# Kernel tuning notes

Measured on AMD Instinct MI355X. Metric: run time of the kernel, lower is better.

## Reference

```python
import jax, jax.numpy as jnp
import numpy as np

B, C, H, W = 32, 3, 256, 256
NGN = 5  # MAX_NUM_OF_GN


def setup_inputs() -> dict:
    key = jax.random.key(0)
    ks = jax.random.split(key, 9)
    f_inp = jax.random.normal(ks[0], (B, C, H, W), jnp.float32)
    # pose: small rotation vector, translation with z ~ 1 (in front of camera)
    rvec = 0.1 * jax.random.normal(ks[1], (B, 3), jnp.float32)
    t_xy = 0.02 * jax.random.normal(ks[2], (B, 2), jnp.float32)
    t_z = 1.0 + 0.2 * jax.random.uniform(ks[3], (B, 1), jnp.float32)
    x_ini = jnp.concatenate([rvec, t_xy, t_z], axis=-1)  # (B,6)
    depth_map = 0.5 + jax.random.uniform(ks[4], (B, H, W), jnp.float32)
    face_index_map = jax.random.randint(ks[5], (B, H, W), 0, 50, jnp.int32) - 1  # -1 = background
    fx = fy = 572.4
    cx, cy = 325.3, 242.0
    Kmat = jnp.array([[fx, 0.0, cx], [0.0, fy, cy], [0.0, 0.0, 1.0]], jnp.float32)
    K = jnp.broadcast_to(Kmat, (B, 3, 3))
    bbox = jax.random.randint(ks[6], (B, 2), 0, 100, jnp.int32).astype(jnp.float32)
    W_pose = 0.1 * jax.random.normal(ks[7], (3, 6), jnp.float32)
    base_feat = jax.random.normal(ks[8], (1, C, H, W), jnp.float32)
    lam = jnp.full((1,), 0.1, jnp.float32)
    return dict(f_inp=f_inp, x_ini=x_ini, depth_map=depth_map,
                face_index_map=face_index_map, K=K, bbox=bbox,
                W_pose=W_pose, base_feat=base_feat, lam=lam)


def _render(x, W_pose, base_feat):
    # surrogate differentiable renderer: pose-conditioned feature map (B,C,H,W)
    return base_feat + jnp.tanh(x @ W_pose.T)[:, :, None, None]


def _spatial_gradient(f):
    # f: (B,C,H,W) -> (B,H,W,C,2) central differences (dx, dy)
    gx = jnp.gradient(f, axis=3)
    gy = jnp.gradient(f, axis=2)
    g = jnp.stack([gx, gy], axis=-1)          # (B,C,H,W,2)
    return jnp.transpose(g, (0, 2, 3, 1, 4))  # (B,H,W,C,2)


def _calculate_jacobian(depth, mask, K, t, bbox):
    # per-pixel 2x6 Jacobian of pixel projection wrt (rot_vec, t); (B,H,W,2,6)
    b, h, w = depth.shape
    fx = K[:, 0, 0][:, None, None]
    fy = K[:, 1, 1][:, None, None]
    cx = K[:, 0, 2][:, None, None]
    cy = K[:, 1, 2][:, None, None]
    u = bbox[:, 0][:, None, None] + jnp.arange(w, dtype=depth.dtype)[None, None, :]
    v = bbox[:, 1][:, None, None] + jnp.arange(h, dtype=depth.dtype)[None, :, None]
    z = depth
    xc = (u - cx) * z / fx            # backprojected camera-frame point
    yc = (v - cy) * z / fy
    zero = jnp.zeros_like(z)
    inv_z = 1.0 / z
    # projection Jacobian wrt camera-frame point: (B,H,W,2,3)
    Jp = jnp.stack([
        jnp.stack([fx * inv_z * jnp.ones_like(z), zero, -fx * xc * inv_z * inv_z], axis=-1),
        jnp.stack([zero, fy * inv_z * jnp.ones_like(z), -fy * yc * inv_z * inv_z], axis=-1),
    ], axis=-2)
    # rotated object point P = X_cam - t ; dX_cam/d(rot_vec) = -[P]_x
    px = xc - t[:, 0][:, None, None]
    py = yc - t[:, 1][:, None, None]
    pz = z - t[:, 2][:, None, None]
    S = jnp.stack([
        jnp.stack([zero, -pz, py], axis=-1),
        jnp.stack([pz, zero, -px], axis=-1),
        jnp.stack([-py, px, zero], axis=-1),
    ], axis=-2)                                       # (B,H,W,3,3)
    J_rot = -jnp.einsum('bhwij,bhwjk->bhwik', Jp, S)  # (B,H,W,2,3)
    Jc = jnp.concatenate([J_rot, Jp], axis=-1)        # (B,H,W,2,6)
    return Jc * mask[..., None, None]


def _gn_step(x, f_inp, depth_map, mask, K, bbox, W_pose, base_feat, damping):
    b = x.shape[0]
    f_rend = _render(x, W_pose, base_feat)                       # (B,C,H,W)
    e = jnp.transpose(f_inp - f_rend, (0, 2, 3, 1)).reshape(b, -1)  # (B, H*W*C)
    grad_xy = _spatial_gradient(f_rend)                          # (B,H,W,C,2)
    Jc = _calculate_jacobian(depth_map, mask, K, x[:, 3:], bbox)  # (B,H,W,2,6)
    J = jnp.einsum('bhwcx,bhwxs->bhwcs', grad_xy, Jc)            # (B,H,W,C,6)
    Jf = J.reshape(b, -1, 6)                                     # (B, H*W*C, 6)
    JtJ = jnp.einsum('bnc,bnd->bcd', Jf, Jf) + damping * jnp.eye(6, dtype=x.dtype)
    Jte = jnp.einsum('bnc,bn->bc', Jf, e)
    dx = jnp.linalg.solve(JtJ, Jte[..., None])[..., 0]
    return x + dx


def reference(f_inp, x_ini, depth_map, face_index_map, K, bbox, W_pose, base_feat, lam):
    mask = (face_index_map >= 0).astype(f_inp.dtype)  # valid rendered pixels
    damping = jax.nn.softplus(lam[0]) + 1e-6
    x = x_ini
    for _ in range(NGN):
        x = _gn_step(x, f_inp, depth_map, mask, K, bbox, W_pose, base_feat, damping)
    return x  # (B,6): refined (rot_vec, t)
```

## Files before the change

kernel.cpp:

```cpp
#include <hip/hip_runtime.h>
#include <math.h>

#define BATCH 32
#define CCH 3
#define HH 256
#define WW 256
#define HW (HH*WW)
#define NGN_IT 5
#define NM 45
#define TROWS 4
#define NTILE (HH/TROWS)
#define NTHR 256
#define NROWCP 38

__host__ __device__ constexpr int idxA(int i, int j) { return 6*i - i*(i+1)/2 + j; }

typedef __attribute__((address_space(1))) const unsigned int gu32;
typedef __attribute__((address_space(3))) unsigned int lu32;

__device__ __forceinline__ void gload_lds16(const float* g, float* l) {
    __builtin_amdgcn_global_load_lds((gu32*)g, (lu32*)l, 16, 0, 0);
}

template<int CTRL, int RMASK, int BMASK>
__device__ __forceinline__ float dpp_add(float x) {
    const int y = __builtin_amdgcn_update_dpp(0, __float_as_int(x), CTRL, RMASK, BMASK, true);
    return x + __int_as_float(y);
}
__device__ __forceinline__ float wave_sum(float x) {
    x = dpp_add<0x111, 0xf, 0xf>(x);
    x = dpp_add<0x112, 0xf, 0xf>(x);
    x = dpp_add<0x114, 0xf, 0xe>(x);
    x = dpp_add<0x118, 0xf, 0xc>(x);
    x = dpp_add<0x142, 0xa, 0xf>(x);
    x = dpp_add<0x143, 0xc, 0xf>(x);
    return x;
}

__global__ __launch_bounds__(NTHR, 4) void k_moments(
    const float* __restrict__ f_inp, const float* __restrict__ depth,
    const int* __restrict__ fidx, const float* __restrict__ Kmat,
    const float* __restrict__ bbox, const float* __restrict__ base_feat,
    float* __restrict__ partials)
{
    const int b   = blockIdx.y;
    const int h0  = blockIdx.x * TROWS;
    const int tid = threadIdx.x;

    __shared__ float bf_s [CCH][TROWS+2][WW];
    __shared__ float fin_s[CCH][TROWS][WW];
    __shared__ float dpt_s[TROWS][WW];
    __shared__ int   msk_s[TROWS][WW];
    __shared__ float red[4*NM];

    const int wv = tid >> 6, ln = tid & 63;

    for (int o = wv; o < NROWCP; o += 4) {
        const float* src; float* dst;
        if (o < 18) {
            const int c = o / 6, k = o % 6;
            int srow = h0 - 1 + k;
            srow = srow < 0 ? 0 : (srow > HH-1 ? HH-1 : srow);
            src = base_feat + ((size_t)c*HH + srow)*WW;
            dst = &bf_s[c][k][0];
        } else if (o < 30) {
            const int t = o - 18, c = t >> 2, r = t & 3;
            src = f_inp + (size_t)b*CCH*HW + ((size_t)c*HH + h0 + r)*WW;
            dst = &fin_s[c][r][0];
        } else if (o < 34) {
            const int r = o - 30;
            src = depth + (size_t)b*HW + (size_t)(h0 + r)*WW;
            dst = &dpt_s[r][0];
        } else {
            const int r = o - 34;
            src = (const float*)(fidx + (size_t)b*HW + (size_t)(h0 + r)*WW);
            dst = (float*)&msk_s[r][0];
        }
        gload_lds16(src + ln*4, dst);
    }

    const float fxv = Kmat[b*9+0], fyv = Kmat[b*9+4];
    const float cx  = Kmat[b*9+2], cy  = Kmat[b*9+5];
    const float bb0 = bbox[b*2+0], bb1 = bbox[b*2+1];
    const float ifx = __builtin_amdgcn_rcpf(fxv);
    const float ify = __builtin_amdgcn_rcpf(fyv);

    __syncthreads();

    const int lp = tid * 4;
    const int lr = lp >> 8;
    const int w0 = lp & (WW-1);
    const int h  = h0 + lr;

    const float4 zv = *(const float4*)&dpt_s[lr][w0];
    const int4   mv = *(const int4*)&msk_s[lr][w0];
    float iz[4];
    iz[0] = __builtin_amdgcn_rcpf(zv.x);
    iz[1] = __builtin_amdgcn_rcpf(zv.y);
    iz[2] = __builtin_amdgcn_rcpf(zv.z);
    iz[3] = __builtin_amdgcn_rcpf(zv.w);
    float mq[4];
    mq[0] = mv.x >= 0 ? 1.f : 0.f; mq[1] = mv.y >= 0 ? 1.f : 0.f;
    mq[2] = mv.z >= 0 ? 1.f : 0.f; mq[3] = mv.w >= 0 ? 1.f : 0.f;

    const float dv_ = bb1 + (float)h - cy;
    const float sy  = (h == 0 || h == HH-1) ? 1.0f : 0.5f;
    const float dvf = dv_*ify;
    const float r02 = -fxv*dvf;
    const float r10 = -(fyv + dv_*dvf);
    const float dvx = dv_*ifx;
    const float fyx = fyv*ifx;
    const float duB = bb0 + (float)w0 - cx;
    const float sx0 = (w0 == 0)    ? 1.0f : 0.5f;
    const float sx3 = (w0 == WW-4) ? 1.0f : 0.5f;
    const int wl = (w0 == 0)    ? 0    : w0-1;
    const int wr = (w0 == WW-4) ? WW-1 : w0+4;

    float acc[NM];
    #pragma unroll
    for (int k = 0; k < NM; ++k) acc[k] = 0.f;

    #pragma unroll
    for (int c = 0; c < CCH; ++c) {
        const float4 ct = *(const float4*)&bf_s[c][lr+1][w0];
        const float4 up = *(const float4*)&bf_s[c][lr+2][w0];
        const float4 dn = *(const float4*)&bf_s[c][lr  ][w0];
        const float lf = bf_s[c][lr+1][wl];
        const float rt = bf_s[c][lr+1][wr];
        const float4 fvc = *(const float4*)&fin_s[c][lr][w0];
        #pragma unroll
        for (int j = 0; j < 4; ++j) {
            const float gx  = (j==0) ? (ct.y - lf  )*sx0 :
                              (j==1) ? (ct.z - ct.x)*0.5f :
                              (j==2) ? (ct.w - ct.y)*0.5f :
                                       (rt   - ct.z)*sx3;
            const float gyv = ((j==0) ? (up.x - dn.x) :
                               (j==1) ? (up.y - dn.y) :
                               (j==2) ? (up.z - dn.z) :
                                        (up.w - dn.w)) * sy;
            const float fc  = (j==0) ? fvc.x : (j==1) ? fvc.y : (j==2) ? fvc.z : fvc.w;
            const float ctj = (j==0) ? ct.x  : (j==1) ? ct.y  : (j==2) ? ct.z  : ct.w;
            const float d   = fc - ctj;
            const float gxm = gx  * mq[j];
            const float gym = gyv * mq[j];
            const float du  = duB + (float)j;
            const float izj = iz[j];
            float J0[6];
            J0[0] = gxm*(-du*dvf)            + gym*r10;
            J0[1] = gxm*(fxv + du*du*ifx)    + gym*(du*dvx);
            J0[2] = gxm*r02                  + gym*(du*fyx);
            J0[3] = gxm*(fxv*izj);
            J0[4] = gym*(fyv*izj);
            J0[5] = -(gxm*du + gym*dv_)*izj;
            #pragma unroll
            for (int i = 0; i < 6; ++i)
                #pragma unroll
                for (int jj = i; jj < 6; ++jj)
                    acc[idxA(i,jj)] += J0[i]*J0[jj];
            #pragma unroll
            for (int s = 0; s < 6; ++s) acc[21 + s] += J0[s]*d;
            #pragma unroll
            for (int s = 0; s < 6; ++s) acc[27 + c*6 + s] += J0[s];
        }
    }

    #pragma unroll
    for (int k = 0; k < NM; ++k) {
        const float v = wave_sum(acc[k]);
        if (ln == 63) red[wv*NM + k] = v;
    }
    __syncthreads();
    if (tid < NM) {
        float s = red[tid] + red[NM + tid] + red[2*NM + tid] + red[3*NM + tid];
        partials[((size_t)b*NM + tid)*NTILE + blockIdx.x] = s;
    }
}

__global__ __launch_bounds__(64) void k_solve(
    const float* __restrict__ partials,
    const float* __restrict__ x_ini,
    const float* __restrict__ W_pose,
    const float* __restrict__ lam,
    float* __restrict__ out)
{
    const int b = blockIdx.x;
    const int tid = threadIdx.x;
    __shared__ float mom[NM];

    if (tid < NM) {
        const float* p = partials + ((size_t)b*NM + tid)*NTILE;
        double s = 0.0;
        #pragma unroll
        for (int i = 0; i < NTILE; ++i) s += (double)p[i];
        mom[tid] = (float)s;
    }
    __syncthreads();
    if (tid != 0) return;

    float A[6][6];
    for (int i = 0; i < 6; ++i)
        for (int j = i; j < 6; ++j) { float v = mom[idxA(i,j)]; A[i][j] = v; A[j][i] = v; }
    float q0[6];
    for (int s = 0; s < 6; ++s) q0[s] = mom[21 + s];
    float R0[3][6];
    for (int c = 0; c < 3; ++c) for (int s = 0; s < 6; ++s) R0[c][s] = mom[27 + c*6 + s];
    float Wp[3][6];
    for (int c = 0; c < 3; ++c) for (int s = 0; s < 6; ++s) Wp[c][s] = W_pose[c*6 + s];
    float x[6];
    for (int s = 0; s < 6; ++s) x[s] = x_ini[b*6 + s];
    const float damping = log1pf(expf(lam[0])) + 1e-6f;

    for (int it = 0; it < NGN_IT; ++it) {
        float tau[3];
        #pragma unroll
        for (int c = 0; c < 3; ++c) {
            float a = 0.f;
            #pragma unroll
            for (int s = 0; s < 6; ++s) a += x[s]*Wp[c][s];
            tau[c] = tanhf(a);
        }
        const float t0 = x[3], t1 = x[4], t2 = x[5];
        const float S[3][3] = {{0.f, -t2, t1}, {t2, 0.f, -t0}, {-t1, t0, 0.f}};

        float M[6][7];
        float PS[3][3], BS[3][3];
        #pragma unroll
        for (int i = 0; i < 3; ++i)
            #pragma unroll
            for (int j = 0; j < 3; ++j) {
                float s1 = 0.f, s2 = 0.f;
                #pragma unroll
                for (int k = 0; k < 3; ++k) { s1 += A[i][3+k]*S[k][j]; s2 += A[3+i][3+k]*S[k][j]; }
                PS[i][j] = s1; BS[i][j] = s2;
            }
        #pragma unroll
        for (int i = 0; i < 3; ++i)
            #pragma unroll
            for (int j = 0; j < 3; ++j) {
                float st = 0.f;
                #pragma unroll
                for (int k = 0; k < 3; ++k) st += S[k][i]*BS[k][j];
                M[i][j] = A[i][j] + PS[i][j] + PS[j][i] + st;
            }
        #pragma unroll
        for (int i = 0; i < 3; ++i)
            #pragma unroll
            for (int j = 0; j < 3; ++j) {
                float tr = A[i][3+j];
                #pragma unroll
                for (int k = 0; k < 3; ++k) tr += S[k][i]*A[3+k][3+j];
                M[i][3+j] = tr; M[3+j][i] = tr;
            }
        #pragma unroll
        for (int i = 0; i < 3; ++i)
            #pragma unroll
            for (int j = 0; j < 3; ++j) M[3+i][3+j] = A[3+i][3+j];
        #pragma unroll
        for (int d_ = 0; d_ < 6; ++d_) M[d_][d_] += damping;

        float base[6];
        #pragma unroll
        for (int s = 0; s < 6; ++s) {
            float v = q0[s];
            #pragma unroll
            for (int c = 0; c < 3; ++c) v -= tau[c]*R0[c][s];
            base[s] = v;
        }
        #pragma unroll
        for (int s = 0; s < 3; ++s) {
            float v = base[s];
            #pragma unroll
            for (int k = 0; k < 3; ++k) v += S[k][s]*base[3+k];
            M[s][6] = v;
        }
        #pragma unroll
        for (int s = 3; s < 6; ++s) M[s][6] = base[s];

        #pragma unroll
        for (int col = 0; col < 6; ++col) {
            const float inv = 1.0f / M[col][col];
            #pragma unroll
            for (int r = col+1; r < 6; ++r) {
                const float f = M[r][col]*inv;
                #pragma unroll
                for (int cc = col; cc < 7; ++cc) M[r][cc] -= f*M[col][cc];
            }
        }
        float sol[6];
        #pragma unroll
        for (int r = 5; r >= 0; --r) {
            float s = M[r][6];
            #pragma unroll
            for (int cc = r+1; cc < 6; ++cc) s -= M[r][cc]*sol[cc];
            sol[r] = s / M[r][r];
        }
        #pragma unroll
        for (int s = 0; s < 6; ++s) x[s] += sol[s];
    }
    #pragma unroll
    for (int s = 0; s < 6; ++s) out[b*6 + s] = x[s];
}

extern "C" void kernel_launch(void* const* d_in, const int* in_sizes, int n_in,
                              void* d_out, int out_size, void* d_ws, size_t ws_size,
                              hipStream_t stream)
{
    (void)in_sizes; (void)n_in; (void)out_size; (void)ws_size;
    const float* f_inp = (const float*)d_in[0];
    const float* x_ini = (const float*)d_in[1];
    const float* depth = (const float*)d_in[2];
    const int*   fidx  = (const int*)  d_in[3];
    const float* Kmat  = (const float*)d_in[4];
    const float* bbox  = (const float*)d_in[5];
    const float* Wp    = (const float*)d_in[6];
    const float* bfeat = (const float*)d_in[7];
    const float* lam   = (const float*)d_in[8];
    float* out = (float*)d_out;

    float* partials = (float*)d_ws;

    dim3 gB(NTILE, BATCH);
    k_moments<<<gB, NTHR, 0, stream>>>(f_inp, depth, fidx, Kmat, bbox, bfeat, partials);
    k_solve<<<BATCH, 64, 0, stream>>>(partials, x_ini, Wp, lam, out);
}
```

Measured before the change: 33.54 us.

## Replace LDS staging with direct global loads and two quads per thread

Drops the async global-to-LDS staging of base_feat, f_inp, depth and mask rows and the barrier that followed it. Each thread now reads its float4s and stencil neighbours straight from global memory, relying on cache for the halo rows. Each block handles 8 rows in two iterations, which halves the grid and the number of partials k_solve must sum. The cost is redundant neighbour loads served from L1/L2 instead of LDS, and fewer blocks to hide load latency.

New measurement: 131.7 us. +292.5%, slower.

```diff
diff --git a/kernel.cpp b/kernel.cpp
--- a/kernel.cpp
+++ b/kernel.cpp
@@ -8,19 +8,11 @@
 #define HW (HH*WW)
 #define NGN_IT 5
 #define NM 45
-#define TROWS 4
-#define NTILE (HH/TROWS)
+#define NBLK 32
 #define NTHR 256
-#define NROWCP 38
+#define QPT 2
 
 __host__ __device__ constexpr int idxA(int i, int j) { return 6*i - i*(i+1)/2 + j; }
-
-typedef __attribute__((address_space(1))) const unsigned int gu32;
-typedef __attribute__((address_space(3))) unsigned int lu32;
-
-__device__ __forceinline__ void gload_lds16(const float* g, float* l) {
-    __builtin_amdgcn_global_load_lds((gu32*)g, (lu32*)l, 16, 0, 0);
-}
 
 template<int CTRL, int RMASK, int BMASK>
 __device__ __forceinline__ float dpp_add(float x) {
@@ -44,40 +36,11 @@
     float* __restrict__ partials)
 {
     const int b   = blockIdx.y;
-    const int h0  = blockIdx.x * TROWS;
+    const int blk = blockIdx.x;
     const int tid = threadIdx.x;
 
-    __shared__ float bf_s [CCH][TROWS+2][WW];
-    __shared__ float fin_s[CCH][TROWS][WW];
-    __shared__ float dpt_s[TROWS][WW];
-    __shared__ int   msk_s[TROWS][WW];
     __shared__ float red[4*NM];
-
     const int wv = tid >> 6, ln = tid & 63;
-
-    for (int o = wv; o < NROWCP; o += 4) {
-        const float* src; float* dst;
-        if (o < 18) {
-            const int c = o / 6, k = o % 6;
-            int srow = h0 - 1 + k;
-            srow = srow < 0 ? 0 : (srow > HH-1 ? HH-1 : srow);
-            src = base_feat + ((size_t)c*HH + srow)*WW;
-            dst = &bf_s[c][k][0];
-        } else if (o < 30) {
-            const int t = o - 18, c = t >> 2, r = t & 3;
-            src = f_inp + (size_t)b*CCH*HW + ((size_t)c*HH + h0 + r)*WW;
-            dst = &fin_s[c][r][0];
-        } else if (o < 34) {
-            const int r = o - 30;
-            src = depth + (size_t)b*HW + (size_t)(h0 + r)*WW;
-            dst = &dpt_s[r][0];
-        } else {
-            const int r = o - 34;
-            src = (const float*)(fidx + (size_t)b*HW + (size_t)(h0 + r)*WW);
-            dst = (float*)&msk_s[r][0];
-        }
-        gload_lds16(src + ln*4, dst);
-    }
 
     const float fxv = Kmat[b*9+0], fyv = Kmat[b*9+4];
     const float cx  = Kmat[b*9+2], cy  = Kmat[b*9+5];
@@ -85,82 +48,87 @@
     const float ifx = __builtin_amdgcn_rcpf(fxv);
     const float ify = __builtin_amdgcn_rcpf(fyv);
 
-    __syncthreads();
-
-    const int lp = tid * 4;
-    const int lr = lp >> 8;
-    const int w0 = lp & (WW-1);
-    const int h  = h0 + lr;
-
-    const float4 zv = *(const float4*)&dpt_s[lr][w0];
-    const int4   mv = *(const int4*)&msk_s[lr][w0];
-    float iz[4];
-    iz[0] = __builtin_amdgcn_rcpf(zv.x);
-    iz[1] = __builtin_amdgcn_rcpf(zv.y);
-    iz[2] = __builtin_amdgcn_rcpf(zv.z);
-    iz[3] = __builtin_amdgcn_rcpf(zv.w);
-    float mq[4];
-    mq[0] = mv.x >= 0 ? 1.f : 0.f; mq[1] = mv.y >= 0 ? 1.f : 0.f;
-    mq[2] = mv.z >= 0 ? 1.f : 0.f; mq[3] = mv.w >= 0 ? 1.f : 0.f;
-
-    const float dv_ = bb1 + (float)h - cy;
-    const float sy  = (h == 0 || h == HH-1) ? 1.0f : 0.5f;
-    const float dvf = dv_*ify;
-    const float r02 = -fxv*dvf;
-    const float r10 = -(fyv + dv_*dvf);
-    const float dvx = dv_*ifx;
-    const float fyx = fyv*ifx;
-    const float duB = bb0 + (float)w0 - cx;
-    const float sx0 = (w0 == 0)    ? 1.0f : 0.5f;
-    const float sx3 = (w0 == WW-4) ? 1.0f : 0.5f;
-    const int wl = (w0 == 0)    ? 0    : w0-1;
-    const int wr = (w0 == WW-4) ? WW-1 : w0+4;
+    const float* __restrict__ dpt  = depth + (size_t)b*HW;
+    const int*   __restrict__ msk  = fidx  + (size_t)b*HW;
+    const float* __restrict__ finb = f_inp + (size_t)b*CCH*HW;
 
     float acc[NM];
     #pragma unroll
     for (int k = 0; k < NM; ++k) acc[k] = 0.f;
 
-    #pragma unroll
-    for (int c = 0; c < CCH; ++c) {
-        const float4 ct = *(const float4*)&bf_s[c][lr+1][w0];
-        const float4 up = *(const float4*)&bf_s[c][lr+2][w0];
-        const float4 dn = *(const float4*)&bf_s[c][lr  ][w0];
-        const float lf = bf_s[c][lr+1][wl];
-        const float rt = bf_s[c][lr+1][wr];
-        const float4 fvc = *(const float4*)&fin_s[c][lr][w0];
-        #pragma unroll
-        for (int j = 0; j < 4; ++j) {
-            const float gx  = (j==0) ? (ct.y - lf  )*sx0 :
-                              (j==1) ? (ct.z - ct.x)*0.5f :
-                              (j==2) ? (ct.w - ct.y)*0.5f :
-                                       (rt   - ct.z)*sx3;
-            const float gyv = ((j==0) ? (up.x - dn.x) :
-                               (j==1) ? (up.y - dn.y) :
-                               (j==2) ? (up.z - dn.z) :
-                                        (up.w - dn.w)) * sy;
-            const float fc  = (j==0) ? fvc.x : (j==1) ? fvc.y : (j==2) ? fvc.z : fvc.w;
-            const float ctj = (j==0) ? ct.x  : (j==1) ? ct.y  : (j==2) ? ct.z  : ct.w;
-            const float d   = fc - ctj;
-            const float gxm = gx  * mq[j];
-            const float gym = gyv * mq[j];
-            const float du  = duB + (float)j;
-            const float izj = iz[j];
-            float J0[6];
-            J0[0] = gxm*(-du*dvf)            + gym*r10;
-            J0[1] = gxm*(fxv + du*du*ifx)    + gym*(du*dvx);
-            J0[2] = gxm*r02                  + gym*(du*fyx);
-            J0[3] = gxm*(fxv*izj);
-            J0[4] = gym*(fyv*izj);
-            J0[5] = -(gxm*du + gym*dv_)*izj;
-            #pragma unroll
-            for (int i = 0; i < 6; ++i)
-                #pragma unroll
-                for (int jj = i; jj < 6; ++jj)
-                    acc[idxA(i,jj)] += J0[i]*J0[jj];
-            #pragma unroll
-            for (int s = 0; s < 6; ++s) acc[21 + s] += J0[s]*d;
-            #pragma unroll
-            for (int s = 0; s < 6; ++s) acc[27 + c*6 + s] += J0[s];
+    #pragma unroll 1
+    for (int it = 0; it < QPT; ++it) {
+        const int qid = blk*(NTHR*QPT) + it*NTHR + tid;
+        const int p0  = qid * 4;
+        const int h   = p0 >> 8;
+        const int w0  = p0 & (WW-1);
+
+        const float4 zv = *(const float4*)(dpt + p0);
+        const int4   mv = *(const int4*)(msk + p0);
+
+        float iz[4];
+        iz[0] = __builtin_amdgcn_rcpf(zv.x);
+        iz[1] = __builtin_amdgcn_rcpf(zv.y);
+        iz[2] = __builtin_amdgcn_rcpf(zv.z);
+        iz[3] = __builtin_amdgcn_rcpf(zv.w);
+        float mq[4];
+        mq[0] = mv.x >= 0 ? 1.f : 0.f; mq[1] = mv.y >= 0 ? 1.f : 0.f;
+        mq[2] = mv.z >= 0 ? 1.f : 0.f; mq[3] = mv.w >= 0 ? 1.f : 0.f;
+
+        const float dv_ = bb1 + (float)h - cy;
+        const float sy  = (h == 0 || h == HH-1) ? 1.0f : 0.5f;
+        const float dvf = dv_*ify;
+        const float r02 = -fxv*dvf;
+        const float r10 = -(fyv + dv_*dvf);
+        const float dvx = dv_*ifx;
+        const float fyx = fyv*ifx;
+        const float duB = bb0 + (float)w0 - cx;
+        const float sx0 = (w0 == 0)    ? 1.0f : 0.5f;
+        const float sx3 = (w0 == WW-4) ? 1.0f : 0.5f;
+
+        #pragma unroll
+        for (int c = 0; c < CCH; ++c) {
+            const float* __restrict__ bfc = base_feat + (size_t)c*HW;
+            const float4 ct = *(const float4*)(bfc + p0);
+            const float4 up = (h == HH-1) ? ct : *(const float4*)(bfc + p0 + WW);
+            const float4 dn = (h == 0)    ? ct : *(const float4*)(bfc + p0 - WW);
+            const float lf = (w0 == 0)    ? ct.x : bfc[p0 - 1];
+            const float rt = (w0 == WW-4) ? ct.w : bfc[p0 + 4];
+            const float4 fvc = *(const float4*)(finb + (size_t)c*HW + p0);
+            #pragma unroll
+            for (int j = 0; j < 4; ++j) {
+                const float gx  = (j==0) ? (ct.y - lf  )*sx0 :
+                                  (j==1) ? (ct.z - ct.x)*0.5f :
+                                  (j==2) ? (ct.w - ct.y)*0.5f :
+                                           (rt   - ct.z)*sx3;
+                const float gyv = ((j==0) ? (up.x - dn.x) :
+                                   (j==1) ? (up.y - dn.y) :
+                                   (j==2) ? (up.z - dn.z) :
+                                            (up.w - dn.w)) * sy;
+                const float fc  = (j==0) ? fvc.x : (j==1) ? fvc.y : (j==2) ? fvc.z : fvc.w;
+                const float ctj = (j==0) ? ct.x  : (j==1) ? ct.y  : (j==2) ? ct.z  : ct.w;
+                const float d   = fc - ctj;
+                const float gxm = gx  * mq[j];
+                const float gym = gyv * mq[j];
+                const float du  = duB + (float)j;
+                const float izj = iz[j];
+                float J0[6];
+                J0[0] = gxm*(-du*dvf)            + gym*r10;
+                J0[1] = gxm*(fxv + du*du*ifx)    + gym*(du*dvx);
+                J0[2] = gxm*r02                  + gym*(du*fyx);
+                J0[3] = gxm*(fxv*izj);
+                J0[4] = gym*(fyv*izj);
+                J0[5] = -(gxm*du + gym*dv_)*izj;
+                #pragma unroll
+                for (int i = 0; i < 6; ++i)
+                    #pragma unroll
+                    for (int jj = i; jj < 6; ++jj)
+                        acc[idxA(i,jj)] += J0[i]*J0[jj];
+                #pragma unroll
+                for (int s = 0; s < 6; ++s) acc[21 + s] += J0[s]*d;
+                #pragma unroll
+                for (int s = 0; s < 6; ++s) acc[27 + c*6 + s] += J0[s];
+            }
         }
     }
 
@@ -172,7 +140,7 @@
     __syncthreads();
     if (tid < NM) {
         float s = red[tid] + red[NM + tid] + red[2*NM + tid] + red[3*NM + tid];
-        partials[((size_t)b*NM + tid)*NTILE + blockIdx.x] = s;
+        partials[((size_t)b*NM + tid)*NBLK + blk] = s;
     }
 }
 
@@ -188,10 +156,10 @@
     __shared__ float mom[NM];
 
     if (tid < NM) {
-        const float* p = partials + ((size_t)b*NM + tid)*NTILE;
+        const float* p = partials + ((size_t)b*NM + tid)*NBLK;
         double s = 0.0;
         #pragma unroll
-        for (int i = 0; i < NTILE; ++i) s += (double)p[i];
+        for (int i = 0; i < NBLK; ++i) s += (double)p[i];
         mom[tid] = (float)s;
     }
     __syncthreads();
@@ -319,7 +287,7 @@
 
     float* partials = (float*)d_ws;
 
-    dim3 gB(NTILE, BATCH);
+    dim3 gB(NBLK, BATCH);
     k_moments<<<gB, NTHR, 0, stream>>>(f_inp, depth, fidx, Kmat, bbox, bfeat, partials);
     k_solve<<<BATCH, 64, 0, stream>>>(partials, x_ini, Wp, lam, out);
 }
```
